# Performance work log

Hardware: AMD Instinct MI355X
Metric: run time of the kernel (lower is better)

The kernel has to match this reference:

```python
import jax, jax.numpy as jnp
import numpy as np

N_HEAD = 16

def setup_inputs() -> dict:
    key = jax.random.key(0)
    k1, k2, k3 = jax.random.split(key, 3)
    B, S, D = 2, 2048, 1024
    x = jax.random.normal(k1, (B, S, D), dtype=jnp.float32)
    w_attn = jax.random.normal(k2, (D, 3 * D), dtype=jnp.float32) * 0.02
    b_attn = jnp.zeros((3 * D,), dtype=jnp.float32)
    w_proj = jax.random.normal(k3, (D, D), dtype=jnp.float32) * 0.02
    b_proj = jnp.zeros((D,), dtype=jnp.float32)
    return {"x": x, "w_attn": w_attn, "b_attn": b_attn, "w_proj": w_proj, "b_proj": b_proj}

def reference(x, w_attn, b_attn, w_proj, b_proj):
    B, S, D = x.shape
    hd = D // N_HEAD
    qkv = x @ w_attn + b_attn                      # [B,S,3D]
    q, k, v = jnp.split(qkv, 3, axis=-1)
    def heads(t):  # [B,S,D] -> [B,H,S,hd]
        return t.reshape(B, S, N_HEAD, hd).transpose(0, 2, 1, 3)
    q, k, v = heads(q), heads(k), heads(v)
    # NOTE: original forward applies NO scaling and NO causal mask; dropout=eval (identity)
    scores = jnp.einsum('bhqd,bhkd->bhqk', q, k)   # [B,H,S,S]
    probs = jax.nn.softmax(scores, axis=-1)
    out = jnp.einsum('bhqk,bhkd->bhqd', probs, v)  # [B,H,S,hd]
    out = out.transpose(0, 2, 1, 3).reshape(B, S, D)
    return out @ w_proj + b_proj
```

## Files before the change

kernel.cpp:

```cpp
#include <hip/hip_runtime.h>

typedef _Float16 f16;
typedef _Float16 f16x8 __attribute__((ext_vector_type(8)));
typedef _Float16 f16x4 __attribute__((ext_vector_type(4)));
typedef float    f32x4 __attribute__((ext_vector_type(4)));
typedef unsigned int u32;
typedef unsigned int u32x4 __attribute__((ext_vector_type(4)));

#define LOG2E 1.44269504088896340736f
#define EXPC  (13.0f * 1.44269504088896340736f)

__device__ __forceinline__ void gload_lds16(const void* g, void* l) {
  __builtin_amdgcn_global_load_lds(
      (const __attribute__((address_space(1))) void*)g,
      (__attribute__((address_space(3))) void*)l, 16, 0, 0);
}

__device__ __forceinline__ void block_sync() {
  asm volatile("" ::: "memory");
  __builtin_amdgcn_s_barrier();
  asm volatile("" ::: "memory");
}

__global__ void k_cast_x(const float* __restrict__ in, f16* __restrict__ out) {
  int i = blockIdx.x * blockDim.x + threadIdx.x;
  f32x4 v = ((const f32x4*)in)[i];
  f16x4 o;
  o[0] = (f16)v[0]; o[1] = (f16)v[1]; o[2] = (f16)v[2]; o[3] = (f16)v[3];
  ((f16x4*)out)[i] = o;
}

__global__ void k_transpose_cast(const float* __restrict__ in, f16* __restrict__ out,
                                 int R, int C) {
  __shared__ float tile[32][33];
  int c0 = blockIdx.x * 32, r0 = blockIdx.y * 32;
  int tx = threadIdx.x, ty = threadIdx.y;
#pragma unroll
  for (int i = 0; i < 4; i++)
    tile[ty + i * 8][tx] = in[(size_t)(r0 + ty + i * 8) * C + c0 + tx];
  __syncthreads();
#pragma unroll
  for (int i = 0; i < 4; i++)
    out[(size_t)(c0 + ty + i * 8) * R + r0 + tx] = (f16)tile[tx][ty + i * 8];
}

template <int EPI>
__global__ __launch_bounds__(256)
void k_gemm(const f16* __restrict__ A, const f16* __restrict__ BT,
            const float* __restrict__ bias,
            f16* __restrict__ out_qk, f16* __restrict__ out_vT,
            float* __restrict__ out_f) {
  constexpr int K = 1024;
  __shared__ f16 smem[4][128 * 64];
  const int t = threadIdx.x;
  const int l = t & 63;
  const int w = t >> 6;
  const int wm = (w >> 1) * 64;
  const int wn = (w & 1) * 64;
  const int m0 = blockIdx.x * 128;
  const int n0 = blockIdx.y * 128;
  const int lr = l & 15;
  const int lg = l >> 4;
  const int fr8 = lr & 7;

  const int row8g = t >> 3;
  const int scg = (t & 7) ^ (row8g & 7);
  const f16* Ap = A + (size_t)(m0 + row8g) * K + scg * 8;
  const f16* Bp = BT + (size_t)(n0 + row8g) * K + scg * 8;

#define GSTAGE(buf) do { \
    _Pragma("unroll") \
    for (int i2 = 0; i2 < 4; i2++) \
      gload_lds16(Ap + (size_t)(i2 * 32) * K, &smem[buf][(i2 * 256 + t) * 8]); \
    _Pragma("unroll") \
    for (int i2 = 0; i2 < 4; i2++) \
      gload_lds16(Bp + (size_t)(i2 * 32) * K, &smem[2 + buf][(i2 * 256 + t) * 8]); \
    Ap += 64; Bp += 64; } while (0)

  f32x4 acc[4][4] = {};

#define GCOMPUTE(buf) do { \
    _Pragma("unroll") \
    for (int kk = 0; kk < 64; kk += 32) { \
      const int cbase = (kk >> 3) + lg;   \
      f16x8 af[4], bf[4]; \
      _Pragma("unroll") \
      for (int i = 0; i < 4; i++) \
        af[i] = *(const f16x8*)&smem[buf][((wm + i * 16 + lr) * 8 + (cbase ^ fr8)) * 8]; \
      _Pragma("unroll") \
      for (int j = 0; j < 4; j++) \
        bf[j] = *(const f16x8*)&smem[2 + buf][((wn + j * 16 + lr) * 8 + (cbase ^ fr8)) * 8]; \
      _Pragma("unroll") \
      for (int i = 0; i < 4; i++) \
        _Pragma("unroll") \
        for (int j = 0; j < 4; j++) \
          acc[i][j] = __builtin_amdgcn_mfma_f32_16x16x32_f16(af[i], bf[j], acc[i][j], 0, 0, 0); \
    } } while (0)

  GSTAGE(0);
  asm volatile("s_waitcnt vmcnt(0)" ::: "memory");
  block_sync();

  for (int kt = 0; kt < 16; kt += 2) {
    GSTAGE(1);
    GCOMPUTE(0);
    asm volatile("s_waitcnt vmcnt(0)" ::: "memory");
    block_sync();
    if (kt + 2 < 16) GSTAGE(0);
    GCOMPUTE(1);
    asm volatile("s_waitcnt vmcnt(0)" ::: "memory");
    block_sync();
  }
#undef GSTAGE
#undef GCOMPUTE

  if (EPI == 1) {
#pragma unroll
    for (int i = 0; i < 4; i++) {
      int mbase = m0 + wm + i * 16 + (l >> 4) * 4;
#pragma unroll
      for (int j = 0; j < 4; j++) {
        int n = n0 + wn + j * 16 + lr;
        float bv = bias[n];
#pragma unroll
        for (int r = 0; r < 4; r++)
          out_f[(size_t)(mbase + r) * 1024 + n] = acc[i][j][r] + bv;
      }
    }
  } else if (n0 < 2048) {
#pragma unroll
    for (int i = 0; i < 4; i++) {
      int mbase = m0 + wm + i * 16 + (l >> 4) * 4;
#pragma unroll
      for (int j = 0; j < 4; j++) {
        int n = n0 + wn + j * 16 + lr;
        float bv = bias[n];
        float sc = (n0 + wn + j * 16 < 1024) ? LOG2E : 1.0f;
#pragma unroll
        for (int r = 0; r < 4; r++)
          out_qk[(size_t)(mbase + r) * 2048 + n] = (f16)((acc[i][j][r] + bv) * sc);
      }
    }
  } else {
    f16* scr = &smem[0][0];
#pragma unroll
    for (int i = 0; i < 4; i++) {
      int s0 = wm + i * 16 + (l >> 4) * 4;
#pragma unroll
      for (int j = 0; j < 4; j++) {
        int nl = wn + j * 16 + lr;
        float bv = bias[n0 + nl];
        f16x4 pv;
#pragma unroll
        for (int r = 0; r < 4; r++) pv[r] = (f16)(acc[i][j][r] + bv);
        *(f16x4*)&scr[nl * 128 + (s0 ^ ((nl & 15) << 3))] = pv;
      }
    }
    block_sync();
    const int b = m0 >> 11;
    const int sbase = m0 & 2047;
#pragma unroll
    for (int p = 0; p < 8; p++) {
      int nl = (t >> 4) + p * 16;
      int sc = (t & 15) << 3;
      f16x8 vv = *(const f16x8*)&scr[nl * 128 + (sc ^ ((nl & 15) << 3))];
      int ng = (n0 - 2048) + nl;
      int hg = ng >> 6, d = ng & 63;
      *(f16x8*)&out_vT[(((size_t)(b * 16 + hg) * 64 + d) << 11) + sbase + sc] = vv;
    }
  }
}

__global__ __launch_bounds__(256, 4)
void k_attn(const f16* __restrict__ qk, const f16* __restrict__ vT,
            f16* __restrict__ aout) {
  __shared__ f16 Kl[2][64 * 64];
  __shared__ f16 Vl[2][64 * 64];
  const int t = threadIdx.x;
  const int l = t & 63;
  const int w = t >> 6;
  const int lr = l & 15;
  const int lg = l >> 4;
  const int lk = lg * 8;

  const int o  = (blockIdx.x & 7) * 128 + (blockIdx.x >> 3);
  const int qt = o & 31;
  const int bh = o >> 5;
  const int b  = bh >> 4;
  const int h  = bh & 15;
  const int q0 = qt * 64 + w * 16;

  const f16* qp = qk + (size_t)(b * 2048 + q0 + lr) * 2048 + h * 64 + lk;
  f16x8 qf0 = *(const f16x8*)qp;
  f16x8 qf1 = *(const f16x8*)(qp + 32);

  const f16* kg = qk + (size_t)(b * 2048) * 2048 + 1024 + h * 64;
  const f16* vg = vT + (size_t)(bh * 64) * 2048;
  const int row8 = t >> 3;
  const int off0 = row8 * 2048 + (((t & 7) ^ (row8 & 7)) << 3);
  const int off1 = off0 + 32 * 2048;

#define STAGE(B) do { \
    gload_lds16(kg + off0, &Kl[B][t * 8]); \
    gload_lds16(kg + off1, &Kl[B][(256 + t) * 8]); \
    gload_lds16(vg + off0, &Vl[B][t * 8]); \
    gload_lds16(vg + off1, &Vl[B][(256 + t) * 8]); \
    kg += 64 * 2048; vg += 64; } while (0)

  f32x4 oa[4] = {};
  f32x4 ssum = {};
  const f32x4 initc = {-EXPC, -EXPC, -EXPC, -EXPC};
  f16x8 ones;
#pragma unroll
  for (int j = 0; j < 8; j++) ones[j] = (f16)1.0f;

  STAGE(0);
  asm volatile("s_waitcnt vmcnt(0)" ::: "memory");
  block_sync();

#define TILE_BODY(B) do { \
    f32x4 sa[4]; \
    __builtin_amdgcn_s_setprio(1); \
    _Pragma("unroll") \
    for (int c = 0; c < 4; c++) { \
      const int ks = c >> 1, cc = c & 1; \
      const int row = ks * 32 + (lr >> 2) * 8 + (lr & 3) * 2 + cc; \
      const int r7 = row & 7; \
      f16x8 kf0 = *(const f16x8*)&Kl[B][(row * 8 + (lg ^ r7)) * 8]; \
      f16x8 kf1 = *(const f16x8*)&Kl[B][(row * 8 + ((lg + 4) ^ r7)) * 8]; \
      sa[c] = __builtin_amdgcn_mfma_f32_16x16x32_f16(kf0, qf0, initc, 0, 0, 0); \
      sa[c] = __builtin_amdgcn_mfma_f32_16x16x32_f16(kf1, qf1, sa[c], 0, 0, 0); \
    } \
    __builtin_amdgcn_s_setprio(0); \
    _Pragma("unroll") \
    for (int c = 0; c < 4; c++) \
      _Pragma("unroll") \
      for (int r = 0; r < 4; r++) \
        sa[c][r] = exp2f(sa[c][r]); \
    u32 pka[2][4]; \
    _Pragma("unroll") \
    for (int ks = 0; ks < 2; ks++) \
      _Pragma("unroll") \
      for (int u = 0; u < 4; u++) \
        pka[ks][u] = __builtin_bit_cast(u32, \
            __builtin_amdgcn_cvt_pkrtz(sa[2 * ks][u], sa[2 * ks + 1][u])); \
    f16x8 pa0 = __builtin_bit_cast(f16x8, (u32x4){pka[0][0], pka[0][1], pka[0][2], pka[0][3]}); \
    f16x8 pa1 = __builtin_bit_cast(f16x8, (u32x4){pka[1][0], pka[1][1], pka[1][2], pka[1][3]}); \
    __builtin_amdgcn_s_setprio(1); \
    ssum = __builtin_amdgcn_mfma_f32_16x16x32_f16(pa0, ones, ssum, 0, 0, 0); \
    ssum = __builtin_amdgcn_mfma_f32_16x16x32_f16(pa1, ones, ssum, 0, 0, 0); \
    _Pragma("unroll") \
    for (int c4 = 0; c4 < 4; c4++) { \
      const int row = c4 * 16 + lr; \
      const int r7 = row & 7; \
      f16x8 vf0 = *(const f16x8*)&Vl[B][(row * 8 + (lg ^ r7)) * 8]; \
      f16x8 vf1 = *(const f16x8*)&Vl[B][(row * 8 + ((lg + 4) ^ r7)) * 8]; \
      oa[c4] = __builtin_amdgcn_mfma_f32_16x16x32_f16(pa0, vf0, oa[c4], 0, 0, 0); \
      oa[c4] = __builtin_amdgcn_mfma_f32_16x16x32_f16(pa1, vf1, oa[c4], 0, 0, 0); \
    } \
    __builtin_amdgcn_s_setprio(0); \
    asm volatile("s_waitcnt vmcnt(0)" ::: "memory"); \
    block_sync(); } while (0)

  for (int tt = 0; tt < 32; tt += 2) {
    STAGE(1);
    TILE_BODY(0);
    if (tt + 2 < 32) STAGE(0);
    TILE_BODY(1);
  }
#undef STAGE
#undef TILE_BODY

#pragma unroll
  for (int r = 0; r < 4; r++) {
    float ia = 1.0f / ssum[r];
    size_t rowa = (size_t)(b * 2048 + q0 + lg * 4 + r);
#pragma unroll
    for (int c4 = 0; c4 < 4; c4++)
      aout[rowa * 1024 + h * 64 + c4 * 16 + lr] = (f16)(oa[c4][r] * ia);
  }
}

extern "C" void kernel_launch(void* const* d_in, const int* in_sizes, int n_in,
                              void* d_out, int out_size, void* d_ws, size_t ws_size,
                              hipStream_t stream) {
  const float* x      = (const float*)d_in[0];
  const float* w_attn = (const float*)d_in[1];
  const float* b_attn = (const float*)d_in[2];
  const float* w_proj = (const float*)d_in[3];
  const float* b_proj = (const float*)d_in[4];
  float* out = (float*)d_out;

  char* p = (char*)d_ws;
  f16* xh  = (f16*)p;  p += (size_t)4096 * 1024 * 2;
  f16* waT = (f16*)p;  p += (size_t)3072 * 1024 * 2;
  f16* wpT = (f16*)p;  p += (size_t)1024 * 1024 * 2;
  f16* qkb = (f16*)p;  p += (size_t)4096 * 2048 * 2;
  f16* vTb = (f16*)p;  p += (size_t)32 * 64 * 2048 * 2;
  f16* aob = (f16*)p;  p += (size_t)4096 * 1024 * 2;
  if ((size_t)(p - (char*)d_ws) > ws_size) return;

  k_cast_x<<<4096, 256, 0, stream>>>(x, xh);
  k_transpose_cast<<<dim3(96, 32), dim3(32, 8), 0, stream>>>(w_attn, waT, 1024, 3072);
  k_transpose_cast<<<dim3(32, 32), dim3(32, 8), 0, stream>>>(w_proj, wpT, 1024, 1024);
  k_gemm<0><<<dim3(32, 24), 256, 0, stream>>>(xh, waT, b_attn, qkb, vTb, nullptr);
  k_attn<<<1024, 256, 0, stream>>>(qkb, vTb, aob);
  k_gemm<1><<<dim3(32, 8), 256, 0, stream>>>(aob, wpT, b_proj, nullptr, nullptr, out);
}
```

Measured before the change: 121.6 us.

## Software-pipeline PV MFMAs behind next tile's QK and fuse prep kernels

The attention loop now delays each tile's P·V and row-sum MFMAs by one iteration. The V fragments and packed probabilities are kept in registers, so these MFMAs can issue right after the next tile's QK MFMAs and overlap with the exp2 work. The three prep kernels (x cast and two weight transpose-casts) are merged into one launch to cut launch overhead. This costs more live registers (vfr, paP0/1), which may lower occupancy, and it adds prologue and epilogue code.

```diff
diff --git a/kernel.cpp b/kernel.cpp
--- a/kernel.cpp
+++ b/kernel.cpp
@@ -22,19 +22,31 @@
   asm volatile("" ::: "memory");
 }
 
-__global__ void k_cast_x(const float* __restrict__ in, f16* __restrict__ out) {
-  int i = blockIdx.x * blockDim.x + threadIdx.x;
-  f32x4 v = ((const f32x4*)in)[i];
-  f16x4 o;
-  o[0] = (f16)v[0]; o[1] = (f16)v[1]; o[2] = (f16)v[2]; o[3] = (f16)v[3];
-  ((f16x4*)out)[i] = o;
-}
-
-__global__ void k_transpose_cast(const float* __restrict__ in, f16* __restrict__ out,
-                                 int R, int C) {
+__global__ __launch_bounds__(256)
+void k_prep(const float* __restrict__ x, f16* __restrict__ xh,
+            const float* __restrict__ w_attn, f16* __restrict__ waT,
+            const float* __restrict__ w_proj, f16* __restrict__ wpT) {
   __shared__ float tile[32][33];
-  int c0 = blockIdx.x * 32, r0 = blockIdx.y * 32;
-  int tx = threadIdx.x, ty = threadIdx.y;
+  const int bid = blockIdx.x;
+  const int t = threadIdx.x;
+  if (bid < 4096) {
+    int i = bid * 256 + t;
+    f32x4 v = ((const f32x4*)x)[i];
+    f16x4 o;
+    o[0] = (f16)v[0]; o[1] = (f16)v[1]; o[2] = (f16)v[2]; o[3] = (f16)v[3];
+    ((f16x4*)xh)[i] = o;
+    return;
+  }
+  const float* in; f16* out; int R, C, bx, by;
+  if (bid < 4096 + 3072) {
+    int q = bid - 4096; in = w_attn; out = waT; R = 1024; C = 3072;
+    bx = q % 96; by = q / 96;
+  } else {
+    int q = bid - 7168; in = w_proj; out = wpT; R = 1024; C = 1024;
+    bx = q % 32; by = q / 32;
+  }
+  int tx = t & 31, ty = t >> 5;
+  int c0 = bx * 32, r0 = by * 32;
 #pragma unroll
   for (int i = 0; i < 4; i++)
     tile[ty + i * 8][tx] = in[(size_t)(r0 + ty + i * 8) * C + c0 + tx];
@@ -82,7 +94,7 @@
 #define GCOMPUTE(buf) do { \
     _Pragma("unroll") \
     for (int kk = 0; kk < 64; kk += 32) { \
-      const int cbase = (kk >> 3) + lg;   \
+      const int cbase = (kk >> 3) + lg; \
       f16x8 af[4], bf[4]; \
       _Pragma("unroll") \
       for (int i = 0; i < 4; i++) \
@@ -214,11 +226,14 @@
 #pragma unroll
   for (int j = 0; j < 8; j++) ones[j] = (f16)1.0f;
 
+  f16x8 vfr[4][2];
+  f16x8 paP0 = {}, paP1 = {};
+
   STAGE(0);
   asm volatile("s_waitcnt vmcnt(0)" ::: "memory");
   block_sync();
 
-#define TILE_BODY(B) do { \
+#define TILE_BODY(B, DO_PV) do { \
     f32x4 sa[4]; \
     __builtin_amdgcn_s_setprio(1); \
     _Pragma("unroll") \
@@ -231,6 +246,15 @@
       sa[c] = __builtin_amdgcn_mfma_f32_16x16x32_f16(kf0, qf0, initc, 0, 0, 0); \
       sa[c] = __builtin_amdgcn_mfma_f32_16x16x32_f16(kf1, qf1, sa[c], 0, 0, 0); \
     } \
+    if (DO_PV) { \
+      ssum = __builtin_amdgcn_mfma_f32_16x16x32_f16(paP0, ones, ssum, 0, 0, 0); \
+      ssum = __builtin_amdgcn_mfma_f32_16x16x32_f16(paP1, ones, ssum, 0, 0, 0); \
+      _Pragma("unroll") \
+      for (int c4 = 0; c4 < 4; c4++) { \
+        oa[c4] = __builtin_amdgcn_mfma_f32_16x16x32_f16(paP0, vfr[c4][0], oa[c4], 0, 0, 0); \
+        oa[c4] = __builtin_amdgcn_mfma_f32_16x16x32_f16(paP1, vfr[c4][1], oa[c4], 0, 0, 0); \
+      } \
+    } \
     __builtin_amdgcn_s_setprio(0); \
     _Pragma("unroll") \
     for (int c = 0; c < 4; c++) \
@@ -244,32 +268,37 @@
       for (int u = 0; u < 4; u++) \
         pka[ks][u] = __builtin_bit_cast(u32, \
             __builtin_amdgcn_cvt_pkrtz(sa[2 * ks][u], sa[2 * ks + 1][u])); \
-    f16x8 pa0 = __builtin_bit_cast(f16x8, (u32x4){pka[0][0], pka[0][1], pka[0][2], pka[0][3]}); \
-    f16x8 pa1 = __builtin_bit_cast(f16x8, (u32x4){pka[1][0], pka[1][1], pka[1][2], pka[1][3]}); \
-    __builtin_amdgcn_s_setprio(1); \
-    ssum = __builtin_amdgcn_mfma_f32_16x16x32_f16(pa0, ones, ssum, 0, 0, 0); \
-    ssum = __builtin_amdgcn_mfma_f32_16x16x32_f16(pa1, ones, ssum, 0, 0, 0); \
+    paP0 = __builtin_bit_cast(f16x8, (u32x4){pka[0][0], pka[0][1], pka[0][2], pka[0][3]}); \
+    paP1 = __builtin_bit_cast(f16x8, (u32x4){pka[1][0], pka[1][1], pka[1][2], pka[1][3]}); \
     _Pragma("unroll") \
     for (int c4 = 0; c4 < 4; c4++) { \
       const int row = c4 * 16 + lr; \
       const int r7 = row & 7; \
-      f16x8 vf0 = *(const f16x8*)&Vl[B][(row * 8 + (lg ^ r7)) * 8]; \
-      f16x8 vf1 = *(const f16x8*)&Vl[B][(row * 8 + ((lg + 4) ^ r7)) * 8]; \
-      oa[c4] = __builtin_amdgcn_mfma_f32_16x16x32_f16(pa0, vf0, oa[c4], 0, 0, 0); \
-      oa[c4] = __builtin_amdgcn_mfma_f32_16x16x32_f16(pa1, vf1, oa[c4], 0, 0, 0); \
+      vfr[c4][0] = *(const f16x8*)&Vl[B][(row * 8 + (lg ^ r7)) * 8]; \
+      vfr[c4][1] = *(const f16x8*)&Vl[B][(row * 8 + ((lg + 4) ^ r7)) * 8]; \
     } \
-    __builtin_amdgcn_s_setprio(0); \
     asm volatile("s_waitcnt vmcnt(0)" ::: "memory"); \
     block_sync(); } while (0)
 
-  for (int tt = 0; tt < 32; tt += 2) {
-    STAGE(1);
-    TILE_BODY(0);
-    if (tt + 2 < 32) STAGE(0);
-    TILE_BODY(1);
-  }
+  STAGE(1);
+  TILE_BODY(0, 0);
+  for (int tt = 1; tt < 31; tt += 2) {
+    STAGE(0);
+    TILE_BODY(1, 1);
+    if (tt + 2 < 32) STAGE(1);
+    TILE_BODY(0, 1);
+  }
+  TILE_BODY(1, 1);
 #undef STAGE
 #undef TILE_BODY
+
+  ssum = __builtin_amdgcn_mfma_f32_16x16x32_f16(paP0, ones, ssum, 0, 0, 0);
+  ssum = __builtin_amdgcn_mfma_f32_16x16x32_f16(paP1, ones, ssum, 0, 0, 0);
+#pragma unroll
+  for (int c4 = 0; c4 < 4; c4++) {
+    oa[c4] = __builtin_amdgcn_mfma_f32_16x16x32_f16(paP0, vfr[c4][0], oa[c4], 0, 0, 0);
+    oa[c4] = __builtin_amdgcn_mfma_f32_16x16x32_f16(paP1, vfr[c4][1], oa[c4], 0, 0, 0);
+  }
 
 #pragma unroll
   for (int r = 0; r < 4; r++) {
@@ -300,9 +329,7 @@
   f16* aob = (f16*)p;  p += (size_t)4096 * 1024 * 2;
   if ((size_t)(p - (char*)d_ws) > ws_size) return;
 
-  k_cast_x<<<4096, 256, 0, stream>>>(x, xh);
-  k_transpose_cast<<<dim3(96, 32), dim3(32, 8), 0, stream>>>(w_attn, waT, 1024, 3072);
-  k_transpose_cast<<<dim3(32, 32), dim3(32, 8), 0, stream>>>(w_proj, wpT, 1024, 1024);
+  k_prep<<<8192, 256, 0, stream>>>(x, xh, w_attn, waT, w_proj, wpT);
   k_gemm<0><<<dim3(32, 24), 256, 0, stream>>>(xh, waT, b_attn, qkb, vTb, nullptr);
   k_attn<<<1024, 256, 0, stream>>>(qkb, vTb, aob);
   k_gemm<1><<<dim3(32, 8), 256, 0, stream>>>(aob, wpT, b_proj, nullptr, nullptr, out);
```

New measurement: 118.0 us. 3.0% less time.
